# Performance work log

Measured on AMD Instinct MI355X. Metric: run time of the kernel, lower is better.

The kernel has to match this reference:

```python
import jax, jax.numpy as jnp
import numpy as np

B, N, D = 16, 2048, 1024
H, DH = 8, 64
I = H * DH            # 512
L = 64                # num_latents
DEPTH = 6
FF = 4 * D


def setup_inputs() -> dict:
    key = jax.random.key(0)
    ks = jax.random.split(key, 8)
    s = 0.02  # weight scale to keep activations well-conditioned
    return {
        "x": jax.random.normal(ks[0], (B, N, D), jnp.float32),
        "mask": jax.random.randint(ks[1], (B, N), 0, 2, jnp.int32),
        "latents": jax.random.normal(ks[2], (L, D), jnp.float32),
        "ln_m_w": jnp.ones((DEPTH, D), jnp.float32),
        "ln_m_b": jnp.zeros((DEPTH, D), jnp.float32),
        "ln_l_w": jnp.ones((DEPTH, D), jnp.float32),
        "ln_l_b": jnp.zeros((DEPTH, D), jnp.float32),
        "Wq": jax.random.normal(ks[3], (DEPTH, D, I), jnp.float32) * s,
        "Wkv": jax.random.normal(ks[4], (DEPTH, D, 2 * I), jnp.float32) * s,
        "Wo": jax.random.normal(ks[5], (DEPTH, I, D), jnp.float32) * s,
        "ff_ln_w": jnp.ones((DEPTH, D), jnp.float32),
        "ff_ln_b": jnp.zeros((DEPTH, D), jnp.float32),
        "W1": jax.random.normal(ks[6], (DEPTH, D, FF), jnp.float32) * s,
        "W2": jax.random.normal(ks[7], (DEPTH, FF, D), jnp.float32) * s,
        "norm_w": jnp.ones((D,), jnp.float32),
        "norm_b": jnp.zeros((D,), jnp.float32),
    }


def _ln(x, w, b, eps=1e-5):
    mu = x.mean(-1, keepdims=True)
    var = ((x - mu) ** 2).mean(-1, keepdims=True)
    return (x - mu) * jax.lax.rsqrt(var + eps) * w + b


def reference(x, mask, latents, ln_m_w, ln_m_b, ln_l_w, ln_l_b,
              Wq, Wkv, Wo, ff_ln_w, ff_ln_b, W1, W2, norm_w, norm_b):
    b, n, d = x.shape
    Lq = latents.shape[0]
    depth = Wq.shape[0]
    h = H
    dh = Wq.shape[-1] // h
    scale = dh ** -0.5

    x4 = x[:, None]  # b 1 n d  (t = 1 media frame)
    lat = jnp.broadcast_to(latents, (b, 1, Lq, d)).astype(x.dtype)
    # mask==1 means masked-out; latents (L zeros) are always attendable
    fmask = jnp.concatenate([mask, jnp.zeros((b, Lq), mask.dtype)], axis=-1)
    mbool = (fmask == 1)[:, None, None, None, :]  # b 1 1 1 S -> broadcast to b t h i S

    for i in range(depth):
        xn = _ln(x4, ln_m_w[i], ln_m_b[i])
        lnl = _ln(lat, ln_l_w[i], ln_l_b[i])
        q = (lnl @ Wq[i]).reshape(b, 1, Lq, h, dh)
        kv = jnp.concatenate([xn, lnl], axis=-2) @ Wkv[i]  # b 1 S 2I
        k, v = jnp.split(kv, 2, axis=-1)
        S = k.shape[-2]
        k = k.reshape(b, 1, S, h, dh)
        v = v.reshape(b, 1, S, h, dh)
        sim = jnp.einsum('btihd,btjhd->bthij', q, k) * scale
        sim = jnp.where(mbool, -jnp.inf, sim)
        sim = sim - jax.lax.stop_gradient(sim.max(axis=-1, keepdims=True))
        attn = jax.nn.softmax(sim, axis=-1)
        out = jnp.einsum('bthij,btjhd->btihd', attn, v).reshape(b, 1, Lq, h * dh)
        lat = out @ Wo[i] + lat
        hf = jax.nn.gelu(_ln(lat, ff_ln_w[i], ff_ln_b[i]) @ W1[i], approximate=False)
        lat = hf @ W2[i] + lat
    return _ln(lat, norm_w, norm_b)
```

## Files before the change

### kernel.cpp

```cpp
#include <hip/hip_runtime.h>

typedef unsigned short u16;
typedef unsigned int u32;
typedef __attribute__((ext_vector_type(8))) short short8;
typedef __attribute__((ext_vector_type(4))) float f4;

#define DEV static __device__ __forceinline__

constexpr int BB = 16, NN = 2048, DD = 1024, HH = 8, DHD = 64, II = 512, LL = 64, DEPTHC = 6, FFC = 4096;

DEV u16 f2bf(float f) {
  union { float f; u32 u; } v; v.f = f;
  u32 r = v.u + 0x7FFFu + ((v.u >> 16) & 1u);
  return (u16)(r >> 16);
}

typedef const u32 __attribute__((address_space(1)))* gas_p;
typedef u32 __attribute__((address_space(3)))* las_p;
DEV void gl_lds16(const void* g, void* l) {
  __builtin_amdgcn_global_load_lds((gas_p)g, (las_p)l, 16, 0, 0);
}

__global__ __launch_bounds__(256) void maskscan_k(const int* __restrict__ mask,
    int* __restrict__ idx, int* __restrict__ cnt) {
  int b = blockIdx.x, tid = threadIdx.x;
  int lane = tid & 63, wv = tid >> 6;
  const int* mrow = mask + (size_t)b * NN;
  int base = tid * 8;
  int keep[8]; int local = 0;
  #pragma unroll
  for (int j = 0; j < 8; j++) { keep[j] = (mrow[base + j] == 0); local += keep[j]; }
  int incl = local;
  #pragma unroll
  for (int off = 1; off < 64; off <<= 1) {
    int v = __shfl_up(incl, off, 64);
    if (lane >= off) incl += v;
  }
  __shared__ int wsum[4];
  if (lane == 63) wsum[wv] = incl;
  __syncthreads();
  int wbase = 0;
  for (int w = 0; w < wv; w++) wbase += wsum[w];
  int pos = wbase + incl - local;
  #pragma unroll
  for (int j = 0; j < 8; j++) if (keep[j]) idx[(size_t)b * NN + pos++] = base + j;
  if (tid == 255) cnt[b] = wbase + incl;
}

__global__ __launch_bounds__(256) void ln_gather_k(const float* __restrict__ x,
    const int* __restrict__ idx, const int* __restrict__ cnt, u16* __restrict__ xcomp) {
  int b = blockIdx.y, j = blockIdx.x, tid = threadIdx.x;
  int c = cnt[b];
  if (j >= ((c + 127) & ~127)) return;
  ushort4* orow = (ushort4*)(xcomp + ((size_t)b * NN + j) * DD);
  if (j >= c) { orow[tid] = make_ushort4(0, 0, 0, 0); return; }
  int src = idx[(size_t)b * NN + j];
  const float4* rp = (const float4*)(x + ((size_t)b * NN + src) * DD);
  float4 v = rp[tid];
  float s = v.x + v.y + v.z + v.w;
  float s2 = v.x*v.x + v.y*v.y + v.z*v.z + v.w*v.w;
  #pragma unroll
  for (int off = 32; off >= 1; off >>= 1) {
    s  += __shfl_xor(s, off, 64);
    s2 += __shfl_xor(s2, off, 64);
  }
  __shared__ float red[8];
  int wv = tid >> 6;
  if ((tid & 63) == 0) { red[wv] = s; red[4 + wv] = s2; }
  __syncthreads();
  s  = red[0] + red[1] + red[2] + red[3];
  s2 = red[4] + red[5] + red[6] + red[7];
  float mu = s * (1.f / DD);
  float var = s2 * (1.f / DD) - mu * mu;
  float rstd = rsqrtf(var + 1e-5f);
  orow[tid] = make_ushort4(f2bf((v.x - mu) * rstd), f2bf((v.y - mu) * rstd),
                           f2bf((v.z - mu) * rstd), f2bf((v.w - mu) * rstd));
}

template<bool OUTF32>
__global__ __launch_bounds__(256) void ln_rows_k(const float* __restrict__ in,
    const float* __restrict__ w, const float* __restrict__ bias, void* __restrict__ out) {
  int row = blockIdx.x;
  int tid = threadIdx.x;
  const float4* rp = (const float4*)(in + (size_t)row * DD);
  float4 x = rp[tid];
  float s = x.x + x.y + x.z + x.w;
  float s2 = x.x*x.x + x.y*x.y + x.z*x.z + x.w*x.w;
  #pragma unroll
  for (int off = 32; off >= 1; off >>= 1) {
    s  += __shfl_xor(s, off, 64);
    s2 += __shfl_xor(s2, off, 64);
  }
  __shared__ float red[8];
  int wv = tid >> 6;
  if ((tid & 63) == 0) { red[wv] = s; red[4 + wv] = s2; }
  __syncthreads();
  s  = red[0] + red[1] + red[2] + red[3];
  s2 = red[4] + red[5] + red[6] + red[7];
  float mu = s * (1.f / DD);
  float var = s2 * (1.f / DD) - mu * mu;
  float rstd = rsqrtf(var + 1e-5f);
  float y[4] = {x.x, x.y, x.z, x.w};
  int col = tid * 4;
  #pragma unroll
  for (int j = 0; j < 4; j++)
    y[j] = (y[j] - mu) * rstd * w[col + j] + bias[col + j];
  if (OUTF32) {
    float4 o = {y[0], y[1], y[2], y[3]};
    ((float4*)out)[(size_t)row * (DD/4) + tid] = o;
  } else {
    ushort4 o = make_ushort4(f2bf(y[0]), f2bf(y[1]), f2bf(y[2]), f2bf(y[3]));
    ((ushort4*)out)[(size_t)row * (DD/4) + tid] = o;
  }
}

__global__ __launch_bounds__(256) void lat_init_k(const float* __restrict__ latents, float* __restrict__ lat) {
  int idx = blockIdx.x * 256 + threadIdx.x;
  ((float4*)lat)[idx] = ((const float4*)latents)[idx & (LL * DD / 4 - 1)];
}

__global__ void zero_k(float* __restrict__ p, int n) {
  int i = blockIdx.x * 256 + threadIdx.x;
  if (i < n) p[i] = 0.f;
}

__global__ void transpall_k(const float* __restrict__ WqA, const float* __restrict__ WkvA,
    const float* __restrict__ WoA, const float* __restrict__ W1A, const float* __restrict__ W2A,
    const float* __restrict__ lnwA, const float* __restrict__ lnbA,
    u16* __restrict__ WqkvTA, u16* __restrict__ WkvTfA, u16* __restrict__ WoTA,
    u16* __restrict__ W1TA, u16* __restrict__ W2TA, float* __restrict__ biaskvA) {
  __shared__ float t[32][33];
  __shared__ float bred[8][32];
  int gid = blockIdx.x;
  int depth = gid / 10240;
  int id = gid % 10240;
  const float* in; u16* o1; int R, C, c0, r0;
  bool iskv = false;
  if (id < 512)       { in = WqA  + (size_t)depth*1024*512;  R = 1024; C = 512;  int l = id;        c0 = (l % 16) * 32;  r0 = (l / 16) * 32;  o1 = WqkvTA + (size_t)depth*1536*1024; }
  else if (id < 1536) { in = WkvA + (size_t)depth*1024*1024; R = 1024; C = 1024; int l = id - 512;  c0 = (l % 32) * 32;  r0 = (l / 32) * 32;  o1 = WqkvTA + (size_t)depth*1536*1024 + 512*1024; iskv = true; }
  else if (id < 2048) { in = WoA  + (size_t)depth*512*1024;  R = 512;  C = 1024; int l = id - 1536; c0 = (l % 32) * 32;  r0 = (l / 32) * 32;  o1 = WoTA + (size_t)depth*1024*512; }
  else if (id < 6144) { in = W1A  + (size_t)depth*1024*4096; R = 1024; C = 4096; int l = id - 2048; c0 = (l % 128) * 32; r0 = (l / 128) * 32; o1 = W1TA + (size_t)depth*4096*1024; }
  else                { in = W2A  + (size_t)depth*4096*1024; R = 4096; C = 1024; int l = id - 6144; c0 = (l % 32) * 32;  r0 = (l / 32) * 32;  o1 = W2TA + (size_t)depth*1024*4096; }
  int tx = threadIdx.x, ty = threadIdx.y;
  #pragma unroll
  for (int j = 0; j < 4; j++)
    t[ty + j*8][tx] = in[(size_t)(r0 + ty + j*8) * C + c0 + tx];
  __syncthreads();
  #pragma unroll
  for (int j = 0; j < 4; j++)
    o1[(size_t)(c0 + ty + j*8) * R + r0 + tx] = f2bf(t[tx][ty + j*8]);
  if (iskv) {
    const float* lnw = lnwA + depth * 1024;
    const float* lnb = lnbA + depth * 1024;
    u16* WkvTf = WkvTfA + (size_t)depth*1024*1024;
    float sc = lnw[r0 + tx];
    #pragma unroll
    for (int j = 0; j < 4; j++)
      WkvTf[(size_t)(c0 + ty + j*8) * 1024 + r0 + tx] = f2bf(t[tx][ty + j*8] * sc);
    float partial = 0.f;
    #pragma unroll
    for (int rr = 0; rr < 4; rr++)
      partial += lnb[r0 + ty + rr*8] * t[ty + rr*8][tx];
    bred[ty][tx] = partial;
    __syncthreads();
    if (ty == 0) {
      float sum = 0.f;
      #pragma unroll
      for (int w = 0; w < 8; w++) sum += bred[w][tx];
      atomicAdd(&biaskvA[depth*1024 + c0 + tx], sum);
    }
  }
}

__global__ __launch_bounds__(256) void gemm_fused_k(
    const u16* __restrict__ xcomp, const u16* __restrict__ WkvTf,
    u16* __restrict__ kvk, u16* __restrict__ vT,
    const float* __restrict__ bias, const int* __restrict__ cnt,
    const u16* __restrict__ lnl, const u16* __restrict__ WqkvT, u16* __restrict__ qkv) {
  __shared__ __align__(16) u16 As[128 * 32];
  __shared__ __align__(16) u16 Bs[128 * 32];
  int id = blockIdx.x;
  int tid = threadIdx.x;
  int wv = tid >> 6, lane = tid & 63;
  const u16 *A, *B;
  int m0, n0, batch = 0, ml = 0;
  bool iskv;
  if (id < 2048) {
    int xg = id & 7, t = id >> 3;
    int mtile = xg * 32 + (t >> 3);
    n0 = (t & 7) * 128;
    batch = mtile >> 4;
    ml = (mtile & 15) * 128;
    if (ml >= cnt[batch]) return;
    m0 = batch * NN + ml;
    A = xcomp; B = WkvTf; iskv = true;
  } else {
    int l = id - 2048;
    m0 = (l / 12) * 128; n0 = (l % 12) * 128;
    A = lnl; B = WqkvT; iskv = false;
  }
  const int K = 1024;
  int srow = wv * 16 + (lane >> 2);
  int scol = (lane & 3) * 8;
  const u16* gA0 = A + (size_t)(m0 + srow) * K + scol;
  const u16* gA1 = A + (size_t)(m0 + 64 + srow) * K + scol;
  const u16* gB0 = B + (size_t)(n0 + srow) * K + scol;
  const u16* gB1 = B + (size_t)(n0 + 64 + srow) * K + scol;
  u16* lA0 = &As[srow * 32 + scol];
  u16* lA1 = &As[(64 + srow) * 32 + scol];
  u16* lB0 = &Bs[srow * 32 + scol];
  u16* lB1 = &Bs[(64 + srow) * 32 + scol];
  int wm = (wv & 1) * 64, wn = (wv >> 1) * 64;
  int fr = lane & 15, fq = (lane >> 4) * 8;
  f4 acc[4][4];
  #pragma unroll
  for (int mi = 0; mi < 4; mi++)
    #pragma unroll
    for (int ni = 0; ni < 4; ni++) acc[mi][ni] = f4{0.f, 0.f, 0.f, 0.f};

  for (int k0 = 0; k0 < K; k0 += 32) {
    gl_lds16(gA0 + k0, lA0);
    gl_lds16(gA1 + k0, lA1);
    gl_lds16(gB0 + k0, lB0);
    gl_lds16(gB1 + k0, lB1);
    __syncthreads();
    short8 af[4], bfr[4];
    #pragma unroll
    for (int mi = 0; mi < 4; mi++)
      af[mi] = *(const short8*)&As[(wm + mi*16 + fr) * 32 + fq];
    #pragma unroll
    for (int ni = 0; ni < 4; ni++)
      bfr[ni] = *(const short8*)&Bs[(wn + ni*16 + fr) * 32 + fq];
    #pragma unroll
    for (int mi = 0; mi < 4; mi++)
      #pragma unroll
      for (int ni = 0; ni < 4; ni++)
        acc[mi][ni] = __builtin_amdgcn_mfma_f32_16x16x32_bf16(af[mi], bfr[ni], acc[mi][ni], 0, 0, 0);
    __syncthreads();
  }
  int er = (lane >> 4) * 4;
  int ec = lane & 15;
  if (iskv) {
    #pragma unroll
    for (int mi = 0; mi < 4; mi++) {
      int rbase = wm + mi*16 + er;
      #pragma unroll
      for (int ni = 0; ni < 4; ni++) {
        int col = n0 + wn + ni*16 + ec;
        float bv = bias[col];
        if (col < 512) {
          #pragma unroll
          for (int r = 0; r < 4; r++)
            kvk[(size_t)(m0 + rbase + r) * 512 + col] = f2bf(acc[mi][ni][r] + bv);
        } else {
          int d = col - 512;
          int hh = d >> 6, dl = d & 63;
          ushort4 o4;
          o4.x = f2bf(acc[mi][ni][0] + bv);
          o4.y = f2bf(acc[mi][ni][1] + bv);
          o4.z = f2bf(acc[mi][ni][2] + bv);
          o4.w = f2bf(acc[mi][ni][3] + bv);
          *(ushort4*)(vT + ((size_t)((batch * 8 + hh) * 64 + dl)) * NN + (ml + rbase)) = o4;
        }
      }
    }
  } else {
    #pragma unroll
    for (int mi = 0; mi < 4; mi++)
      #pragma unroll
      for (int ni = 0; ni < 4; ni++) {
        int col = n0 + wn + ni*16 + ec;
        #pragma unroll
        for (int r = 0; r < 4; r++) {
          int row = m0 + wm + mi*16 + er + r;
          qkv[(size_t)row * 1536 + col] = f2bf(acc[mi][ni][r]);
        }
      }
  }
}

__global__ __launch_bounds__(256) void gemm_gelu_k(const u16* __restrict__ A, const u16* __restrict__ Bm,
    u16* __restrict__ C, int M, int N, int K) {
  __shared__ __align__(16) u16 As[128 * 32];
  __shared__ __align__(16) u16 Bs[64 * 32];
  int tid = threadIdx.x;
  int wv = tid >> 6, lane = tid & 63;
  int m0 = blockIdx.y * 128, n0 = blockIdx.x * 64;
  int srow = wv * 16 + (lane >> 2);
  int scol = (lane & 3) * 8;
  const u16* gA0 = A + (size_t)(m0 + srow) * K + scol;
  const u16* gA1 = A + (size_t)(m0 + 64 + srow) * K + scol;
  const u16* gB0 = Bm + (size_t)(n0 + srow) * K + scol;
  u16* lA0 = &As[srow * 32 + scol];
  u16* lA1 = &As[(64 + srow) * 32 + scol];
  u16* lB0 = &Bs[srow * 32 + scol];
  int wm = (wv & 1) * 64, wn = (wv >> 1) * 32;
  int fr = lane & 15, fq = (lane >> 4) * 8;
  f4 acc[4][2];
  #pragma unroll
  for (int mi = 0; mi < 4; mi++)
    #pragma unroll
    for (int ni = 0; ni < 2; ni++) acc[mi][ni] = f4{0.f, 0.f, 0.f, 0.f};

  for (int k0 = 0; k0 < K; k0 += 32) {
    gl_lds16(gA0 + k0, lA0);
    gl_lds16(gA1 + k0, lA1);
    gl_lds16(gB0 + k0, lB0);
    __syncthreads();
    short8 af[4], bfr[2];
    #pragma unroll
    for (int mi = 0; mi < 4; mi++)
      af[mi] = *(const short8*)&As[(wm + mi*16 + fr) * 32 + fq];
    #pragma unroll
    for (int ni = 0; ni < 2; ni++)
      bfr[ni] = *(const short8*)&Bs[(wn + ni*16 + fr) * 32 + fq];
    #pragma unroll
    for (int mi = 0; mi < 4; mi++)
      #pragma unroll
      for (int ni = 0; ni < 2; ni++)
        acc[mi][ni] = __builtin_amdgcn_mfma_f32_16x16x32_bf16(af[mi], bfr[ni], acc[mi][ni], 0, 0, 0);
    __syncthreads();
  }
  int er = (lane >> 4) * 4;
  int ec = lane & 15;
  #pragma unroll
  for (int mi = 0; mi < 4; mi++)
    #pragma unroll
    for (int ni = 0; ni < 2; ni++) {
      int col = n0 + wn + ni*16 + ec;
      #pragma unroll
      for (int r = 0; r < 4; r++) {
        int row = m0 + wm + mi*16 + er + r;
        float v = acc[mi][ni][r];
        v = 0.5f * v * (1.f + erff(v * 0.70710678118654752f));
        C[(size_t)row * N + col] = f2bf(v);
      }
    }
}

__global__ __launch_bounds__(256) void gemmsk_k(const u16* __restrict__ A, const u16* __restrict__ Bm,
    float* __restrict__ C, int M, int N, int K, int Kc) {
  __shared__ __align__(16) u16 As[128 * 32];
  __shared__ __align__(16) u16 Bs[64 * 32];
  int tid = threadIdx.x;
  int wv = tid >> 6, lane = tid & 63;
  int m0 = blockIdx.y * 128, n0 = blockIdx.x * 64;
  int kb = blockIdx.z * Kc;
  int srow = wv * 16 + (lane >> 2);
  int scol = (lane & 3) * 8;
  const u16* gA0 = A + (size_t)(m0 + srow) * K + kb + scol;
  const u16* gA1 = A + (size_t)(m0 + 64 + srow) * K + kb + scol;
  const u16* gB0 = Bm + (size_t)(n0 + srow) * K + kb + scol;
  u16* lA0 = &As[srow * 32 + scol];
  u16* lA1 = &As[(64 + srow) * 32 + scol];
  u16* lB0 = &Bs[srow * 32 + scol];
  int wm = (wv & 1) * 64, wn = (wv >> 1) * 32;
  int fr = lane & 15, fq = (lane >> 4) * 8;
  f4 acc[4][2];
  #pragma unroll
  for (int mi = 0; mi < 4; mi++)
    #pragma unroll
    for (int ni = 0; ni < 2; ni++) acc[mi][ni] = f4{0.f, 0.f, 0.f, 0.f};

  for (int k0 = 0; k0 < Kc; k0 += 32) {
    gl_lds16(gA0 + k0, lA0);
    gl_lds16(gA1 + k0, lA1);
    gl_lds16(gB0 + k0, lB0);
    __syncthreads();
    short8 af[4], bfr[2];
    #pragma unroll
    for (int mi = 0; mi < 4; mi++)
      af[mi] = *(const short8*)&As[(wm + mi*16 + fr) * 32 + fq];
    #pragma unroll
    for (int ni = 0; ni < 2; ni++)
      bfr[ni] = *(const short8*)&Bs[(wn + ni*16 + fr) * 32 + fq];
    #pragma unroll
    for (int mi = 0; mi < 4; mi++)
      #pragma unroll
      for (int ni = 0; ni < 2; ni++)
        acc[mi][ni] = __builtin_amdgcn_mfma_f32_16x16x32_bf16(af[mi], bfr[ni], acc[mi][ni], 0, 0, 0);
    __syncthreads();
  }
  int er = (lane >> 4) * 4;
  int ec = lane & 15;
  #pragma unroll
  for (int mi = 0; mi < 4; mi++)
    #pragma unroll
    for (int ni = 0; ni < 2; ni++) {
      int col = n0 + wn + ni*16 + ec;
      #pragma unroll
      for (int r = 0; r < 4; r++) {
        int row = m0 + wm + mi*16 + er + r;
        atomicAdd(&C[(size_t)row * N + col], acc[mi][ni][r]);
      }
    }
}

__global__ __launch_bounds__(256) void attn_part_k(const u16* __restrict__ qkv,
    const u16* __restrict__ kvk, const u16* __restrict__ vT, const int* __restrict__ cnt,
    float* __restrict__ opart, float* __restrict__ mlpart) {
  int id = blockIdx.x;
  int b = id >> 5;
  int h = (id >> 2) & 7;
  int part = id & 3;
  int tid = threadIdx.x;
  int wv = tid >> 6, lane = tid & 63;
  int fr = lane & 15, fq8 = (lane >> 4) * 8;
  int c = cnt[b];
  int nt = (c + 63) >> 6;
  int T = nt + 1;
  int t0 = (T * part) >> 2;
  int t1 = (T * (part + 1)) >> 2;

  __shared__ __align__(16) u16 ks[64 * 88];
  __shared__ __align__(16) u16 vs[64 * 88];
  __shared__ __align__(16) u16 ps[4][16 * 88];
  __shared__ float smask[64];

  const u16* qp = qkv + (size_t)(b * LL + wv * 16 + fr) * 1536 + h * DHD;
  short8 aq0 = *(const short8*)(qp + fq8);
  short8 aq1 = *(const short8*)(qp + 32 + fq8);

  float m_i[4], l_i[4];
  f4 o[4];
  #pragma unroll
  for (int r = 0; r < 4; r++) { m_i[r] = -1e30f; l_i[r] = 0.f; }
  #pragma unroll
  for (int dt = 0; dt < 4; dt++) o[dt] = f4{0.f, 0.f, 0.f, 0.f};

  const float scale = 0.125f;

  for (int t = t0; t < t1; t++) {
    bool isLat = (t == nt);
    __syncthreads();
    if (isLat) {
      const u16* src = qkv + (size_t)(b * LL) * 1536 + 512 + h * DHD;
      #pragma unroll
      for (int it = 0; it < 2; it++) {
        int cid = it * 256 + tid;
        int kr = cid >> 3, c8 = (cid & 7) * 8;
        int4 kvv = *(const int4*)(src + (size_t)kr * 1536 + c8);
        *(int4*)&ks[kr * 88 + c8] = kvv;
        int4 vvv = *(const int4*)(src + 512 + (size_t)kr * 1536 + c8);
        const u16* ve = (const u16*)&vvv;
        #pragma unroll
        for (int j = 0; j < 8; j++) vs[(c8 + j) * 88 + kr] = ve[j];
      }
    } else {
      const u16* ksrc = kvk + (size_t)(b * NN + t * 64) * 512 + h * DHD;
      const u16* vsrc = vT + (size_t)((b * 8 + h) * 64) * NN + t * 64;
      #pragma unroll
      for (int it = 0; it < 2; it++) {
        int cid = it * 256 + tid;
        int kr = cid >> 3, c8 = (cid & 7) * 8;
        *(int4*)&ks[kr * 88 + c8] = *(const int4*)(ksrc + (size_t)kr * 512 + c8);
        *(int4*)&vs[kr * 88 + c8] = *(const int4*)(vsrc + (size_t)kr * NN + c8);
      }
    }
    if (tid < 64)
      smask[tid] = (isLat || (t * 64 + tid < c)) ? 0.f : -1e30f;
    __syncthreads();

    f4 sim[4];
    #pragma unroll
    for (int ct = 0; ct < 4; ct++) {
      short8 b0 = *(const short8*)&ks[(ct*16 + fr) * 88 + fq8];
      short8 b1 = *(const short8*)&ks[(ct*16 + fr) * 88 + 32 + fq8];
      f4 s = f4{0.f, 0.f, 0.f, 0.f};
      s = __builtin_amdgcn_mfma_f32_16x16x32_bf16(aq0, b0, s, 0, 0, 0);
      s = __builtin_amdgcn_mfma_f32_16x16x32_bf16(aq1, b1, s, 0, 0, 0);
      float mk = smask[ct*16 + fr];
      #pragma unroll
      for (int r = 0; r < 4; r++) s[r] = s[r] * scale + mk;
      sim[ct] = s;
    }
    float mnew[4], alpha[4], p[4][4];
    #pragma unroll
    for (int r = 0; r < 4; r++) {
      float mx = fmaxf(fmaxf(sim[0][r], sim[1][r]), fmaxf(sim[2][r], sim[3][r]));
      #pragma unroll
      for (int off = 8; off >= 1; off >>= 1) mx = fmaxf(mx, __shfl_xor(mx, off, 16));
      mnew[r] = fmaxf(m_i[r], mx);
      alpha[r] = __expf(m_i[r] - mnew[r]);
      m_i[r] = mnew[r];
      float ssum = 0.f;
      #pragma unroll
      for (int ct = 0; ct < 4; ct++) { float e = __expf(sim[ct][r] - mnew[r]); p[ct][r] = e; ssum += e; }
      #pragma unroll
      for (int off = 8; off >= 1; off >>= 1) ssum += __shfl_xor(ssum, off, 16);
      l_i[r] = l_i[r] * alpha[r] + ssum;
    }
    #pragma unroll
    for (int ct = 0; ct < 4; ct++)
      #pragma unroll
      for (int r = 0; r < 4; r++)
        ps[wv][((lane>>4)*4 + r) * 88 + ct*16 + fr] = f2bf(p[ct][r]);
    #pragma unroll
    for (int dt = 0; dt < 4; dt++)
      #pragma unroll
      for (int r = 0; r < 4; r++) o[dt][r] *= alpha[r];
    short8 pa0 = *(const short8*)&ps[wv][fr * 88 + fq8];
    short8 pa1 = *(const short8*)&ps[wv][fr * 88 + 32 + fq8];
    #pragma unroll
    for (int dt = 0; dt < 4; dt++) {
      short8 bv0 = *(const short8*)&vs[(dt*16 + fr) * 88 + fq8];
      short8 bv1 = *(const short8*)&vs[(dt*16 + fr) * 88 + 32 + fq8];
      o[dt] = __builtin_amdgcn_mfma_f32_16x16x32_bf16(pa0, bv0, o[dt], 0, 0, 0);
      o[dt] = __builtin_amdgcn_mfma_f32_16x16x32_bf16(pa1, bv1, o[dt], 0, 0, 0);
    }
  }
  #pragma unroll
  for (int dt = 0; dt < 4; dt++)
    #pragma unroll
    for (int r = 0; r < 4; r++) {
      int row = wv * 16 + (lane>>4)*4 + r;
      int col = dt*16 + fr;
      opart[((size_t)id * 64 + row) * 64 + col] = o[dt][r];
    }
  if (fr == 0) {
    #pragma unroll
    for (int r = 0; r < 4; r++) {
      int row = wv * 16 + (lane>>4)*4 + r;
      mlpart[id * 128 + row * 2]     = m_i[r];
      mlpart[id * 128 + row * 2 + 1] = l_i[r];
    }
  }
}

__global__ __launch_bounds__(256) void attn_comb_k(const float* __restrict__ opart,
    const float* __restrict__ mlpart, u16* __restrict__ out) {
  int bh = blockIdx.x;
  int b = bh >> 3, h = bh & 7;
  int tid = threadIdx.x;
  int row = tid >> 2;
  int c0 = (tid & 3) * 16;
  float mp[4], lp[4];
  float m = -1e30f;
  #pragma unroll
  for (int p = 0; p < 4; p++) {
    mp[p] = mlpart[(bh * 4 + p) * 128 + row * 2];
    lp[p] = mlpart[(bh * 4 + p) * 128 + row * 2 + 1];
    m = fmaxf(m, mp[p]);
  }
  float a[4]; float L = 0.f;
  #pragma unroll
  for (int p = 0; p < 4; p++) { a[p] = __expf(mp[p] - m); L += lp[p] * a[p]; }
  float rl = 1.f / L;
  u16* op = out + ((size_t)(b * LL + row)) * II + h * DHD + c0;
  #pragma unroll
  for (int j = 0; j < 4; j++) {
    float acc4[4] = {0.f, 0.f, 0.f, 0.f};
    #pragma unroll
    for (int p = 0; p < 4; p++) {
      const float4* pp = (const float4*)(opart + ((size_t)(bh * 4 + p) * 64 + row) * 64 + c0);
      float4 v = pp[j];
      acc4[0] += v.x * a[p]; acc4[1] += v.y * a[p];
      acc4[2] += v.z * a[p]; acc4[3] += v.w * a[p];
    }
    op[j*4 + 0] = f2bf(acc4[0] * rl);
    op[j*4 + 1] = f2bf(acc4[1] * rl);
    op[j*4 + 2] = f2bf(acc4[2] * rl);
    op[j*4 + 3] = f2bf(acc4[3] * rl);
  }
}

extern "C" void kernel_launch(void* const* d_in, const int* in_sizes, int n_in,
                              void* d_out, int out_size, void* d_ws, size_t ws_size,
                              hipStream_t stream) {
  (void)in_sizes; (void)n_in; (void)out_size; (void)ws_size;
  const float* x       = (const float*)d_in[0];
  const int*   mask    = (const int*)d_in[1];
  const float* latents = (const float*)d_in[2];
  const float* ln_m_w  = (const float*)d_in[3];
  const float* ln_m_b  = (const float*)d_in[4];
  const float* ln_l_w  = (const float*)d_in[5];
  const float* ln_l_b  = (const float*)d_in[6];
  const float* Wq      = (const float*)d_in[7];
  const float* Wkv     = (const float*)d_in[8];
  const float* Wo      = (const float*)d_in[9];
  const float* ff_ln_w = (const float*)d_in[10];
  const float* ff_ln_b = (const float*)d_in[11];
  const float* W1      = (const float*)d_in[12];
  const float* W2      = (const float*)d_in[13];
  const float* norm_w  = (const float*)d_in[14];
  const float* norm_b  = (const float*)d_in[15];
  float* out = (float*)d_out;

  char* ws = (char*)d_ws;
  size_t off = 0;
  auto alloc = [&](size_t bytes) -> void* {
    void* p = ws + off; off += (bytes + 255) & ~(size_t)255; return p;
  };
  u16* xcomp = (u16*)alloc((size_t)32768 * 1024 * 2);
  u16* kvk   = (u16*)alloc((size_t)32768 * 512 * 2);
  u16* vT    = (u16*)alloc((size_t)8192 * 2048 * 2);
  int* idxb  = (int*)alloc((size_t)32768 * 4);
  int* cnt   = (int*)alloc(64);
  float* lat = (float*)alloc((size_t)1024 * 1024 * 4);
  u16* lnl   = (u16*)alloc((size_t)1024 * 1024 * 2);
  u16* latn  = (u16*)alloc((size_t)1024 * 1024 * 2);
  u16* qkv   = (u16*)alloc((size_t)1024 * 1536 * 2);
  u16* aout  = (u16*)alloc((size_t)1024 * 512 * 2);
  u16* hf    = (u16*)alloc((size_t)1024 * 4096 * 2);
  float* opart  = (float*)alloc((size_t)512 * 64 * 64 * 4);
  float* mlpart = (float*)alloc((size_t)512 * 128 * 4);
  u16* WqkvT = (u16*)alloc((size_t)DEPTHC * 1536 * 1024 * 2);
  u16* WkvTf = (u16*)alloc((size_t)DEPTHC * 1024 * 1024 * 2);
  u16* WoT   = (u16*)alloc((size_t)DEPTHC * 1024 * 512 * 2);
  u16* W1T   = (u16*)alloc((size_t)DEPTHC * 4096 * 1024 * 2);
  u16* W2T   = (u16*)alloc((size_t)DEPTHC * 1024 * 4096 * 2);
  float* biaskv_all = (float*)alloc(DEPTHC * 1024 * 4);

  maskscan_k<<<16, 256, 0, stream>>>(mask, idxb, cnt);
  ln_gather_k<<<dim3(2048, 16), 256, 0, stream>>>(x, idxb, cnt, xcomp);
  lat_init_k<<<1024, 256, 0, stream>>>(latents, lat);
  zero_k<<<24, 256, 0, stream>>>(biaskv_all, DEPTHC * 1024);
  transpall_k<<<DEPTHC * 10240, dim3(32, 8), 0, stream>>>(
      Wq, Wkv, Wo, W1, W2, ln_m_w, ln_m_b,
      WqkvT, WkvTf, WoT, W1T, W2T, biaskv_all);

  for (int i = 0; i < DEPTHC; i++) {
    ln_rows_k<false><<<1024, 256, 0, stream>>>(lat, ln_l_w + i*1024, ln_l_b + i*1024, lnl);
    gemm_fused_k<<<2144, 256, 0, stream>>>(
        xcomp, WkvTf + (size_t)i*1024*1024, kvk, vT, biaskv_all + i*1024, cnt,
        lnl, WqkvT + (size_t)i*1536*1024, qkv);
    attn_part_k<<<512, 256, 0, stream>>>(qkv, kvk, vT, cnt, opart, mlpart);
    attn_comb_k<<<128, 256, 0, stream>>>(opart, mlpart, aout);
    gemmsk_k<<<dim3(16, 8, 4), 256, 0, stream>>>(aout, WoT + (size_t)i*1024*512, lat, 1024, 1024, 512, 128);
    ln_rows_k<false><<<1024, 256, 0, stream>>>(lat, ff_ln_w + i*1024, ff_ln_b + i*1024, latn);
    gemm_gelu_k<<<dim3(64, 8), 256, 0, stream>>>(latn, W1T + (size_t)i*4096*1024, hf, 1024, 4096, 1024);
    gemmsk_k<<<dim3(16, 8, 4), 256, 0, stream>>>(hf, W2T + (size_t)i*1024*4096, lat, 1024, 1024, 4096, 1024);
  }
  ln_rows_k<true><<<1024, 256, 0, stream>>>(lat, norm_w, norm_b, out);
}
```

Measured before the change: 1.493 ms.

## Vectorize weight transpose with 64x64 tiles and split attention into eight parts

The weight transpose/convert kernel now uses 64x64 tiles with float4 loads and packed 16-byte bf16 stores, and reduces the kv bias partial sums with wave shuffles instead of a shared-memory reduction. This cuts the number of blocks and the count of narrow memory transactions in the one-time weight preprocessing. Separately, the split-KV attention now uses 8 partitions per (batch, head) instead of 4, doubling the grid to 1024 blocks for better CU occupancy. The combine kernel reads twice as many partial results in exchange.

New measurement: 1.527 ms. 1.02x slower.

```diff
diff --git a/kernel.cpp b/kernel.cpp
--- a/kernel.cpp
+++ b/kernel.cpp
@@ -13,6 +13,10 @@
   union { float f; u32 u; } v; v.f = f;
   u32 r = v.u + 0x7FFFu + ((v.u >> 16) & 1u);
   return (u16)(r >> 16);
+}
+
+DEV u32 pack2(float lo, float hi) {
+  return (u32)f2bf(lo) | ((u32)f2bf(hi) << 16);
 }
 
 typedef const u32 __attribute__((address_space(1)))* gas_p;
@@ -124,50 +128,68 @@
   if (i < n) p[i] = 0.f;
 }
 
-__global__ void transpall_k(const float* __restrict__ WqA, const float* __restrict__ WkvA,
+__global__ __launch_bounds__(256) void transpall_k(const float* __restrict__ WqA, const float* __restrict__ WkvA,
     const float* __restrict__ WoA, const float* __restrict__ W1A, const float* __restrict__ W2A,
     const float* __restrict__ lnwA, const float* __restrict__ lnbA,
     u16* __restrict__ WqkvTA, u16* __restrict__ WkvTfA, u16* __restrict__ WoTA,
     u16* __restrict__ W1TA, u16* __restrict__ W2TA, float* __restrict__ biaskvA) {
-  __shared__ float t[32][33];
-  __shared__ float bred[8][32];
+  __shared__ float t[64][65];
   int gid = blockIdx.x;
-  int depth = gid / 10240;
-  int id = gid % 10240;
+  int depth = gid / 2560;
+  int id = gid % 2560;
   const float* in; u16* o1; int R, C, c0, r0;
   bool iskv = false;
-  if (id < 512)       { in = WqA  + (size_t)depth*1024*512;  R = 1024; C = 512;  int l = id;        c0 = (l % 16) * 32;  r0 = (l / 16) * 32;  o1 = WqkvTA + (size_t)depth*1536*1024; }
-  else if (id < 1536) { in = WkvA + (size_t)depth*1024*1024; R = 1024; C = 1024; int l = id - 512;  c0 = (l % 32) * 32;  r0 = (l / 32) * 32;  o1 = WqkvTA + (size_t)depth*1536*1024 + 512*1024; iskv = true; }
-  else if (id < 2048) { in = WoA  + (size_t)depth*512*1024;  R = 512;  C = 1024; int l = id - 1536; c0 = (l % 32) * 32;  r0 = (l / 32) * 32;  o1 = WoTA + (size_t)depth*1024*512; }
-  else if (id < 6144) { in = W1A  + (size_t)depth*1024*4096; R = 1024; C = 4096; int l = id - 2048; c0 = (l % 128) * 32; r0 = (l / 128) * 32; o1 = W1TA + (size_t)depth*4096*1024; }
-  else                { in = W2A  + (size_t)depth*4096*1024; R = 4096; C = 1024; int l = id - 6144; c0 = (l % 32) * 32;  r0 = (l / 32) * 32;  o1 = W2TA + (size_t)depth*1024*4096; }
-  int tx = threadIdx.x, ty = threadIdx.y;
-  #pragma unroll
-  for (int j = 0; j < 4; j++)
-    t[ty + j*8][tx] = in[(size_t)(r0 + ty + j*8) * C + c0 + tx];
-  __syncthreads();
-  #pragma unroll
-  for (int j = 0; j < 4; j++)
-    o1[(size_t)(c0 + ty + j*8) * R + r0 + tx] = f2bf(t[tx][ty + j*8]);
+  if (id < 128)       { in = WqA  + (size_t)depth*1024*512;  R = 1024; C = 512;  int l = id;        c0 = (l & 7) * 64;  r0 = (l >> 3) * 64; o1 = WqkvTA + (size_t)depth*1536*1024; }
+  else if (id < 384)  { in = WkvA + (size_t)depth*1024*1024; R = 1024; C = 1024; int l = id - 128;  c0 = (l & 15) * 64; r0 = (l >> 4) * 64; o1 = WqkvTA + (size_t)depth*1536*1024 + 512*1024; iskv = true; }
+  else if (id < 512)  { in = WoA  + (size_t)depth*512*1024;  R = 512;  C = 1024; int l = id - 384;  c0 = (l & 15) * 64; r0 = (l >> 4) * 64; o1 = WoTA + (size_t)depth*1024*512; }
+  else if (id < 1536) { in = W1A  + (size_t)depth*1024*4096; R = 1024; C = 4096; int l = id - 512;  c0 = (l & 63) * 64; r0 = (l >> 6) * 64; o1 = W1TA + (size_t)depth*4096*1024; }
+  else                { in = W2A  + (size_t)depth*4096*1024; R = 4096; C = 1024; int l = id - 1536; c0 = (l & 15) * 64; r0 = (l >> 4) * 64; o1 = W2TA + (size_t)depth*1024*4096; }
+  int tid = threadIdx.x;
+  int lr = tid >> 4, lc4 = (tid & 15) * 4;
+  #pragma unroll
+  for (int p = 0; p < 4; p++) {
+    int row = p * 16 + lr;
+    float4 v = *(const float4*)&in[(size_t)(r0 + row) * C + c0 + lc4];
+    t[row][lc4] = v.x; t[row][lc4+1] = v.y; t[row][lc4+2] = v.z; t[row][lc4+3] = v.w;
+  }
+  int oc = tid >> 3;
+  int rg = tid & 7;
+  float lw[8], lb[8];
   if (iskv) {
     const float* lnw = lnwA + depth * 1024;
     const float* lnb = lnbA + depth * 1024;
-    u16* WkvTf = WkvTfA + (size_t)depth*1024*1024;
-    float sc = lnw[r0 + tx];
-    #pragma unroll
-    for (int j = 0; j < 4; j++)
-      WkvTf[(size_t)(c0 + ty + j*8) * 1024 + r0 + tx] = f2bf(t[tx][ty + j*8] * sc);
-    float partial = 0.f;
-    #pragma unroll
-    for (int rr = 0; rr < 4; rr++)
-      partial += lnb[r0 + ty + rr*8] * t[ty + rr*8][tx];
-    bred[ty][tx] = partial;
-    __syncthreads();
-    if (ty == 0) {
-      float sum = 0.f;
-      #pragma unroll
-      for (int w = 0; w < 8; w++) sum += bred[w][tx];
-      atomicAdd(&biaskvA[depth*1024 + c0 + tx], sum);
+    int rbase = r0 + rg * 8;
+    float4 w0 = *(const float4*)&lnw[rbase];
+    float4 w1 = *(const float4*)&lnw[rbase + 4];
+    float4 b0 = *(const float4*)&lnb[rbase];
+    float4 b1 = *(const float4*)&lnb[rbase + 4];
+    lw[0]=w0.x; lw[1]=w0.y; lw[2]=w0.z; lw[3]=w0.w; lw[4]=w1.x; lw[5]=w1.y; lw[6]=w1.z; lw[7]=w1.w;
+    lb[0]=b0.x; lb[1]=b0.y; lb[2]=b0.z; lb[3]=b0.w; lb[4]=b1.x; lb[5]=b1.y; lb[6]=b1.z; lb[7]=b1.w;
+  }
+  __syncthreads();
+  #pragma unroll
+  for (int p = 0; p < 2; p++) {
+    int c = p * 32 + oc;
+    float v[8];
+    #pragma unroll
+    for (int k = 0; k < 8; k++) v[k] = t[rg * 8 + k][c];
+    int4 o;
+    o.x = (int)pack2(v[0], v[1]); o.y = (int)pack2(v[2], v[3]);
+    o.z = (int)pack2(v[4], v[5]); o.w = (int)pack2(v[6], v[7]);
+    *(int4*)&o1[(size_t)(c0 + c) * R + r0 + rg * 8] = o;
+    if (iskv) {
+      u16* WkvTf = WkvTfA + (size_t)depth*1024*1024;
+      int4 of;
+      of.x = (int)pack2(v[0]*lw[0], v[1]*lw[1]); of.y = (int)pack2(v[2]*lw[2], v[3]*lw[3]);
+      of.z = (int)pack2(v[4]*lw[4], v[5]*lw[5]); of.w = (int)pack2(v[6]*lw[6], v[7]*lw[7]);
+      *(int4*)&WkvTf[(size_t)(c0 + c) * 1024 + r0 + rg * 8] = of;
+      float partial = 0.f;
+      #pragma unroll
+      for (int k = 0; k < 8; k++) partial += lb[k] * v[k];
+      partial += __shfl_xor(partial, 1, 64);
+      partial += __shfl_xor(partial, 2, 64);
+      partial += __shfl_xor(partial, 4, 64);
+      if (rg == 0) atomicAdd(&biaskvA[depth*1024 + c0 + c], partial);
     }
   }
 }
@@ -400,17 +422,17 @@
     const u16* __restrict__ kvk, const u16* __restrict__ vT, const int* __restrict__ cnt,
     float* __restrict__ opart, float* __restrict__ mlpart) {
   int id = blockIdx.x;
-  int b = id >> 5;
-  int h = (id >> 2) & 7;
-  int part = id & 3;
+  int b = id >> 6;
+  int h = (id >> 3) & 7;
+  int part = id & 7;
   int tid = threadIdx.x;
   int wv = tid >> 6, lane = tid & 63;
   int fr = lane & 15, fq8 = (lane >> 4) * 8;
   int c = cnt[b];
   int nt = (c + 63) >> 6;
   int T = nt + 1;
-  int t0 = (T * part) >> 2;
-  int t1 = (T * (part + 1)) >> 2;
+  int t0 = (T * part) >> 3;
+  int t1 = (T * (part + 1)) >> 3;
 
   __shared__ __align__(16) u16 ks[64 * 88];
   __shared__ __align__(16) u16 vs[64 * 88];
@@ -534,25 +556,25 @@
   int tid = threadIdx.x;
   int row = tid >> 2;
   int c0 = (tid & 3) * 16;
-  float mp[4], lp[4];
+  float mp[8], lp[8];
   float m = -1e30f;
   #pragma unroll
-  for (int p = 0; p < 4; p++) {
-    mp[p] = mlpart[(bh * 4 + p) * 128 + row * 2];
-    lp[p] = mlpart[(bh * 4 + p) * 128 + row * 2 + 1];
+  for (int p = 0; p < 8; p++) {
+    mp[p] = mlpart[(bh * 8 + p) * 128 + row * 2];
+    lp[p] = mlpart[(bh * 8 + p) * 128 + row * 2 + 1];
     m = fmaxf(m, mp[p]);
   }
-  float a[4]; float L = 0.f;
-  #pragma unroll
-  for (int p = 0; p < 4; p++) { a[p] = __expf(mp[p] - m); L += lp[p] * a[p]; }
+  float a[8]; float L = 0.f;
+  #pragma unroll
+  for (int p = 0; p < 8; p++) { a[p] = __expf(mp[p] - m); L += lp[p] * a[p]; }
   float rl = 1.f / L;
   u16* op = out + ((size_t)(b * LL + row)) * II + h * DHD + c0;
   #pragma unroll
   for (int j = 0; j < 4; j++) {
     float acc4[4] = {0.f, 0.f, 0.f, 0.f};
     #pragma unroll
-    for (int p = 0; p < 4; p++) {
-      const float4* pp = (const float4*)(opart + ((size_t)(bh * 4 + p) * 64 + row) * 64 + c0);
+    for (int p = 0; p < 8; p++) {
+      const float4* pp = (const float4*)(opart + ((size_t)(bh * 8 + p) * 64 + row) * 64 + c0);
       float4 v = pp[j];
       acc4[0] += v.x * a[p]; acc4[1] += v.y * a[p];
       acc4[2] += v.z * a[p]; acc4[3] += v.w * a[p];
@@ -602,8 +624,8 @@
   u16* qkv   = (u16*)alloc((size_t)1024 * 1536 * 2);
   u16* aout  = (u16*)alloc((size_t)1024 * 512 * 2);
   u16* hf    = (u16*)alloc((size_t)1024 * 4096 * 2);
-  float* opart  = (float*)alloc((size_t)512 * 64 * 64 * 4);
-  float* mlpart = (float*)alloc((size_t)512 * 128 * 4);
+  float* opart  = (float*)alloc((size_t)1024 * 64 * 64 * 4);
+  float* mlpart = (float*)alloc((size_t)1024 * 128 * 4);
   u16* WqkvT = (u16*)alloc((size_t)DEPTHC * 1536 * 1024 * 2);
   u16* WkvTf = (u16*)alloc((size_t)DEPTHC * 1024 * 1024 * 2);
   u16* WoT   = (u16*)alloc((size_t)DEPTHC * 1024 * 512 * 2);
@@ -615,7 +637,7 @@
   ln_gather_k<<<dim3(2048, 16), 256, 0, stream>>>(x, idxb, cnt, xcomp);
   lat_init_k<<<1024, 256, 0, stream>>>(latents, lat);
   zero_k<<<24, 256, 0, stream>>>(biaskv_all, DEPTHC * 1024);
-  transpall_k<<<DEPTHC * 10240, dim3(32, 8), 0, stream>>>(
+  transpall_k<<<DEPTHC * 2560, 256, 0, stream>>>(
       Wq, Wkv, Wo, W1, W2, ln_m_w, ln_m_b,
       WqkvT, WkvTf, WoT, W1T, W2T, biaskv_all);
 
@@ -624,7 +646,7 @@
     gemm_fused_k<<<2144, 256, 0, stream>>>(
         xcomp, WkvTf + (size_t)i*1024*1024, kvk, vT, biaskv_all + i*1024, cnt,
         lnl, WqkvT + (size_t)i*1536*1024, qkv);
-    attn_part_k<<<512, 256, 0, stream>>>(qkv, kvk, vT, cnt, opart, mlpart);
+    attn_part_k<<<1024, 256, 0, stream>>>(qkv, kvk, vT, cnt, opart, mlpart);
     attn_comb_k<<<128, 256, 0, stream>>>(opart, mlpart, aout);
     gemmsk_k<<<dim3(16, 8, 4), 256, 0, stream>>>(aout, WoT + (size_t)i*1024*512, lat, 1024, 1024, 512, 128);
     ln_rows_k<false><<<1024, 256, 0, stream>>>(lat, ff_ln_w + i*1024, ff_ln_b + i*1024, latn);
```
